# Kernel tuning notes

Measured on AMD Instinct MI355X. Metric: run time of the kernel, lower is better.

The kernel has to match this reference:

```python
import jax, jax.numpy as jnp
import numpy as np

B, D_IN, D, D_OUT, N_BLOCKS = 32768, 100, 1024, 1, 5
H = 0.1
EPS = 1e-4


def setup_inputs() -> dict:
    key = jax.random.key(0)
    ks = jax.random.split(key, 10)
    x = jax.random.normal(ks[0], (B, D_IN), dtype=jnp.float32)
    # first linear: D_IN -> D
    W0 = jax.random.normal(ks[1], (D, D_IN), dtype=jnp.float32) / np.sqrt(D_IN)
    b0 = jnp.zeros((D,), dtype=jnp.float32)
    # middle residual linears: D -> D, stacked over blocks
    Ws = jax.random.normal(ks[2], (N_BLOCKS, D, D), dtype=jnp.float32) / np.sqrt(D)
    bs = jnp.zeros((N_BLOCKS, D), dtype=jnp.float32)
    # brownian Linear(D, 1, bias=False) weight vectors, one per block
    bw = jax.random.normal(ks[3], (N_BLOCKS, D), dtype=jnp.float32) / np.sqrt(D)
    # last linear: D -> D_OUT
    Wlast = jax.random.normal(ks[4], (D_OUT, D), dtype=jnp.float32) / np.sqrt(D)
    blast = jnp.zeros((D_OUT,), dtype=jnp.float32)
    # torch.rand_like(out): uniform [0,1) noise per block
    noise = jax.random.uniform(ks[5], (N_BLOCKS, B, D), dtype=jnp.float32)
    return {"x": x, "W0": W0, "b0": b0, "Ws": Ws, "bs": bs,
            "bw": bw, "Wlast": Wlast, "blast": blast, "noise": noise}


def reference(x, W0, b0, Ws, bs, bw, Wlast, blast, noise):
    sqrt_h = H ** 0.5
    out = jnp.tanh(x @ W0.T + b0)  # [B, D]
    for i in range(N_BLOCKS):
        z = noise[i]  # [B, D]
        w = bw[i]     # [D]
        # product(): z @ (w w^T + eps I)^T = (z.w) w + eps z  (rank-1, O(D))
        proj = (z @ w)[:, None] * w + EPS * z
        out = out + H * jnp.tanh(out @ Ws[i].T + bs[i]) + sqrt_h * proj
    return out @ Wlast.T + blast  # [B, D_OUT]
```

## Files before the change

kernel.cpp:

```cpp
#include <hip/hip_runtime.h>
#include <hip/hip_bf16.h>


typedef unsigned short u16;
typedef __attribute__((ext_vector_type(8))) short short8;
typedef __attribute__((ext_vector_type(8))) u16 u16x8;
typedef __attribute__((ext_vector_type(4))) u16 u16x4;
typedef __attribute__((ext_vector_type(4))) float f32x4;

#define BROWS 32768
#define DDIM 1024
#define NBLK 5
#define H_STEP 0.1f
#define SQRT_H 0.31622776601683794f

#define FENCE() asm volatile("" ::: "memory")
#define BARRIER() do { FENCE(); __builtin_amdgcn_s_barrier(); FENCE(); } while (0)

__device__ __forceinline__ float bf2f(u16 u) {
    return __uint_as_float(((unsigned)u) << 16);
}
__device__ __forceinline__ u16 f2bf(float f) {
    unsigned u = __float_as_uint(f);
    unsigned r = 0x7fffu + ((u >> 16) & 1u);
    return (u16)((u + r) >> 16);
}
__device__ __forceinline__ float fast_tanh(float s) {
    float e = __expf(2.0f * s);
    return 1.0f - 2.0f * __builtin_amdgcn_rcpf(e + 1.0f);
}

#define GLOAD_LDS16(g, l)                                                        \
    __builtin_amdgcn_global_load_lds(                                            \
        (const __attribute__((address_space(1))) unsigned int*)(const void*)(g), \
        (__attribute__((address_space(3))) unsigned int*)(void*)(l), 16, 0, 0)

__global__ __launch_bounds__(256) void pad_cvt(const float* __restrict__ src,
                                               u16* __restrict__ dst,
                                               int R, int C, int Cp) {
    int idx = blockIdx.x * 256 + threadIdx.x;
    if (idx >= R * Cp) return;
    int r = idx / Cp;
    int c = idx - r * Cp;
    float v = (c < C) ? src[(size_t)r * C + c] : 0.0f;
    dst[idx] = f2bf(v);
}

__global__ __launch_bounds__(256) void zw_kernel(const float* __restrict__ noise,
                                                 const float* __restrict__ bw,
                                                 float* __restrict__ zw) {
    int gw = (blockIdx.x * 256 + threadIdx.x) >> 6;
    int lane = threadIdx.x & 63;
    if (gw >= NBLK * BROWS) return;
    int i = gw >> 15;
    const float* zr = noise + (size_t)gw * DDIM;
    const float* wr = bw + i * DDIM;
    float s = 0.0f;
#pragma unroll
    for (int it = 0; it < 4; ++it) {
        int k = it * 256 + lane * 4;
        f32x4 z = *(const f32x4*)(zr + k);
        f32x4 w = *(const f32x4*)(wr + k);
        s += z.x * w.x + z.y * w.y + z.z * w.z + z.w * w.w;
    }
#pragma unroll
    for (int off = 32; off > 0; off >>= 1) s += __shfl_down(s, off, 64);
    if (lane == 0) zw[gw] = s;
}

template <int KK, int EPI>
__global__ __launch_bounds__(512, 2) void gemm256(const u16* __restrict__ Ag,
                                                  const u16* __restrict__ Bg,
                                                  const float* __restrict__ bias,
                                                  u16* __restrict__ outW,
                                                  const u16* __restrict__ outR,
                                                  const float* __restrict__ zw,
                                                  const float* __restrict__ bwv) {
    constexpr int NT = KK / 64;
    static_assert(NT >= 2 && (NT & 1) == 0, "NT even, >=2");
    __shared__ __align__(16) u16 smem[65536];
    char* lds = (char*)smem;

    const int bid = blockIdx.x;
    const int swz = (bid & 7) * 64 + (bid >> 3);
    const int row0 = (swz >> 2) * 256;
    const int col0 = (swz & 3) * 256;

    const int tid = threadIdx.x;
    const int lane = tid & 63;
    const int wid = tid >> 6;
    const int wm = wid >> 2;
    const int wn = wid & 3;

    const int srow = tid >> 2;
    const int skq = (tid & 3) ^ ((tid >> 3) & 3);
    const u16* agp0 = Ag + (size_t)(row0 + srow) * KK + skq * 8;
    const u16* agp1 = Ag + (size_t)(row0 + 128 + srow) * KK + skq * 8;
    const u16* bgp0 = Bg + (size_t)(col0 + srow) * KK + skq * 8;
    const u16* bgp1 = Bg + (size_t)(col0 + 128 + srow) * KK + skq * 8;
    char* lp0 = lds + wid * 1024;

    auto stage = [&](int t, int q) {
        const int is_b = q & 1;
        const int kh = q >> 1;
        const int koff = t * 64 + kh * 32;
        char* dst = lp0 + ((t & 1) << 16) + (is_b << 15) + (kh << 14);
        const u16* g0 = (is_b ? bgp0 : agp0) + koff;
        const u16* g1 = (is_b ? bgp1 : agp1) + koff;
        GLOAD_LDS16(g0, dst);
        GLOAD_LDS16(g1, dst + 8192);
    };

    const int rchunk = ((lane >> 4) ^ ((lane >> 1) & 3)) << 4;
    const int aoffL = (wm * 128 + (lane & 15)) * 64 + rchunk;
    const int boffL = 32768 + (wn * 64 + (lane & 15)) * 64 + rchunk;

    short8 af[8], bf[4];
    f32x4 acc[8][4];
#pragma unroll
    for (int m = 0; m < 8; ++m)
#pragma unroll
        for (int n = 0; n < 4; ++n) acc[m][n] = (f32x4){0.f, 0.f, 0.f, 0.f};

#define RD(off) (*(const short8*)(lds + (off)))
#define PHASE2(kh, bufc, STG1, STG2, VMW)                                             \
    do {                                                                              \
        STG1;                                                                         \
        STG2;                                                                         \
        VMW;                                                                          \
        FENCE(); __builtin_amdgcn_s_barrier(); FENCE();                               \
        __builtin_amdgcn_s_setprio(1);                                                \
        const int rb = (bufc) * 65536 + (kh) * 16384;                                 \
        _Pragma("unroll") for (int m = 0; m < 8; ++m)                                 \
            af[m] = RD(rb + aoffL + m * 1024);                                        \
        _Pragma("unroll") for (int n = 0; n < 4; ++n)                                 \
            bf[n] = RD(rb + boffL + n * 1024);                                        \
        _Pragma("unroll") for (int m = 0; m < 8; ++m)                                 \
            _Pragma("unroll") for (int n = 0; n < 4; ++n)                             \
                acc[m][n] = __builtin_amdgcn_mfma_f32_16x16x32_bf16(af[m], bf[n], acc[m][n], 0, 0, 0); \
        __builtin_amdgcn_s_setprio(0);                                                \
        FENCE(); __builtin_amdgcn_s_barrier(); FENCE();                               \
    } while (0)
#define VM4 asm volatile("s_waitcnt vmcnt(4)" ::: "memory")
#define VM0 asm volatile("s_waitcnt vmcnt(0)" ::: "memory")
#define NOSTG ((void)0)
#define NOVM ((void)0)

#define TILE2(t, c)                                                                   \
    do {                                                                              \
        PHASE2(0, c, stage((t) + 1, 2), stage((t) + 1, 3), NOVM);                     \
        PHASE2(1, c, stage((t) + 2, 0), stage((t) + 2, 1), VM4);                      \
    } while (0)

    stage(0, 0); stage(0, 1); stage(0, 2); stage(0, 3);
    stage(1, 0); stage(1, 1);
    asm volatile("s_waitcnt vmcnt(4)" ::: "memory");
    BARRIER();

    for (int t2 = 0; t2 < NT / 2 - 1; ++t2) {
        TILE2(2 * t2, 0);
        TILE2(2 * t2 + 1, 1);
    }
    PHASE2(0, 0, stage(NT - 1, 2), stage(NT - 1, 3), NOVM);
    PHASE2(1, 0, NOSTG, NOSTG, VM0);
    PHASE2(0, 1, NOSTG, NOSTG, NOVM);
    PHASE2(1, 1, NOSTG, NOSTG, NOVM);

    float bcol[4];
#pragma unroll
    for (int ng = 0; ng < 4; ++ng) bcol[ng] = bias[col0 + wn * 64 + ng * 16 + (lane & 15)];

    char* wbase = lds + wid * 16384;
    const int lr0 = (lane >> 4) * 4;
    const int lc0 = lane & 15;
#pragma unroll
    for (int m = 0; m < 8; ++m) {
#pragma unroll
        for (int ng = 0; ng < 4; ++ng) {
#pragma unroll
            for (int j = 0; j < 4; ++j) {
                int lrow = m * 16 + lr0 + j;
                int lcol = ng * 16 + lc0;
                float t = fast_tanh(acc[m][ng][j] + bcol[ng]);
                float d = (EPI == 0) ? t : H_STEP * t;
                int chunk = (lcol >> 3) ^ ((lrow >> 2) & 7);
                *(u16*)(wbase + lrow * 128 + (chunk << 4) + (lcol & 7) * 2) = f2bf(d);
            }
        }
    }

    const int gr_base = row0 + wm * 128;
    const int gc_base = col0 + wn * 64;
#pragma unroll
    for (int it = 0; it < 16; ++it) {
        int lrow = it * 8 + (lane >> 3);
        int chunk = lane & 7;
        int schunk = chunk ^ ((lrow >> 2) & 7);
        u16x8 d8 = *(const u16x8*)(wbase + lrow * 128 + (schunk << 4));
        int grow = gr_base + lrow;
        int gcol = gc_base + chunk * 8;
        size_t gidx = (size_t)grow * DDIM + gcol;
        u16x8 o8;
        if constexpr (EPI == 0) {
            o8 = d8;
        } else {
            u16x8 old8 = *(const u16x8*)(outR + gidx);
            float zr = SQRT_H * zw[grow];
            f32x4 bw0 = *(const f32x4*)(bwv + gcol);
            f32x4 bw1 = *(const f32x4*)(bwv + gcol + 4);
#pragma unroll
            for (int e = 0; e < 8; ++e) {
                float bwe = (e < 4) ? bw0[e] : bw1[e - 4];
                float v = bf2f(old8[e]) + bf2f(d8[e]) + zr * bwe;
                o8[e] = f2bf(v);
            }
        }
        *(u16x8*)(outW + gidx) = o8;
    }
#undef RD
#undef PHASE2
#undef VM4
#undef VM0
#undef NOSTG
#undef NOVM
#undef TILE2
}

__global__ __launch_bounds__(256) void last_k(const u16* __restrict__ out,
                                              const float* __restrict__ wlast,
                                              const float* __restrict__ blast,
                                              float* __restrict__ y) {
    int gw = (blockIdx.x * 256 + threadIdx.x) >> 6;
    int lane = threadIdx.x & 63;
    if (gw >= BROWS) return;
    const u16* orow = out + (size_t)gw * DDIM;
    float s = 0.0f;
#pragma unroll
    for (int it = 0; it < 4; ++it) {
        int k = it * 256 + lane * 4;
        u16x4 o = *(const u16x4*)(orow + k);
        f32x4 w = *(const f32x4*)(wlast + k);
        s += bf2f(o.x) * w.x + bf2f(o.y) * w.y + bf2f(o.z) * w.z + bf2f(o.w) * w.w;
    }
#pragma unroll
    for (int off = 32; off > 0; off >>= 1) s += __shfl_down(s, off, 64);
    if (lane == 0) y[gw] = s + blast[0];
}

extern "C" void kernel_launch(void* const* d_in, const int* in_sizes, int n_in,
                              void* d_out, int out_size, void* d_ws, size_t ws_size,
                              hipStream_t stream) {
    const float* x     = (const float*)d_in[0];
    const float* W0    = (const float*)d_in[1];
    const float* b0    = (const float*)d_in[2];
    const float* Ws    = (const float*)d_in[3];
    const float* bs    = (const float*)d_in[4];
    const float* bw    = (const float*)d_in[5];
    const float* Wlast = (const float*)d_in[6];
    const float* blast = (const float*)d_in[7];
    const float* noise = (const float*)d_in[8];
    float* y = (float*)d_out;
    (void)in_sizes; (void)n_in; (void)out_size; (void)ws_size;

    char* ws = (char*)d_ws;
    size_t off = 0;
    auto alloc = [&](size_t bytes) {
        char* p = ws + off;
        off += (bytes + 255) & ~(size_t)255;
        return p;
    };
    u16* outB0 = (u16*)alloc((size_t)BROWS * DDIM * 2);
    u16* outB1 = (u16*)alloc((size_t)BROWS * DDIM * 2);
    u16* xb    = (u16*)alloc((size_t)BROWS * 128 * 2);
    u16* W0b   = (u16*)alloc((size_t)DDIM * 128 * 2);
    u16* Wsb   = (u16*)alloc((size_t)NBLK * DDIM * DDIM * 2);
    float* zw  = (float*)alloc((size_t)NBLK * BROWS * 4);

    pad_cvt<<<(BROWS * 128 + 255) / 256, 256, 0, stream>>>(x, xb, BROWS, 100, 128);
    pad_cvt<<<(DDIM * 128 + 255) / 256, 256, 0, stream>>>(W0, W0b, DDIM, 100, 128);
    pad_cvt<<<(NBLK * DDIM * DDIM + 255) / 256, 256, 0, stream>>>(Ws, Wsb, NBLK * DDIM, DDIM, DDIM);

    zw_kernel<<<(NBLK * BROWS) / 4, 256, 0, stream>>>(noise, bw, zw);

    gemm256<128, 0><<<512, 512, 0, stream>>>(xb, W0b, b0, outB0,
                                             nullptr, nullptr, nullptr);

    u16* cur = outB0;
    u16* nxt = outB1;
    for (int i = 0; i < NBLK; ++i) {
        gemm256<1024, 1><<<512, 512, 0, stream>>>(
            cur, Wsb + (size_t)i * DDIM * DDIM, bs + (size_t)i * DDIM, nxt, cur,
            zw + (size_t)i * BROWS, bw + (size_t)i * DDIM);
        u16* t = cur; cur = nxt; nxt = t;
    }

    last_k<<<BROWS / 4, 256, 0, stream>>>(cur, Wlast, blast, y);
}
```

Before: 605.8 us.

## Switch GEMM to 32x32x16 MFMA with fragment-contiguous LDS staging layout

Replaces the 16x16x32 bf16 MFMA inner loop with 32x32x16 MFMA tiles (4x2 per wave). It also restages global-to-LDS loads so each 32-row by 16-k fragment sits contiguously, letting each lane read its operand with one linear offset and no swizzle math. This cuts the number of MFMA issues and LDS reads per k-step, aiming for higher matrix-core throughput. The trade-off is a changed LDS layout with possible bank conflicts and a remapped epilogue indexing that must match the 32x32 accumulator layout.

```diff
diff --git a/kernel.cpp b/kernel.cpp
--- a/kernel.cpp
+++ b/kernel.cpp
@@ -7,6 +7,7 @@
 typedef __attribute__((ext_vector_type(8))) u16 u16x8;
 typedef __attribute__((ext_vector_type(4))) u16 u16x4;
 typedef __attribute__((ext_vector_type(4))) float f32x4;
+typedef __attribute__((ext_vector_type(16))) float f32x16;
 
 #define BROWS 32768
 #define DDIM 1024
@@ -92,96 +93,122 @@
     const int wm = wid >> 2;
     const int wn = wid & 3;
 
-    const int srow = tid >> 2;
-    const int skq = (tid & 3) ^ ((tid >> 3) & 3);
-    const u16* agp0 = Ag + (size_t)(row0 + srow) * KK + skq * 8;
-    const u16* agp1 = Ag + (size_t)(row0 + 128 + srow) * KK + skq * 8;
-    const u16* bgp0 = Bg + (size_t)(col0 + srow) * KK + skq * 8;
-    const u16* bgp1 = Bg + (size_t)(col0 + 128 + srow) * KK + skq * 8;
-    char* lp0 = lds + wid * 1024;
-
-    auto stage = [&](int t, int q) {
-        const int is_b = q & 1;
-        const int kh = q >> 1;
-        const int koff = t * 64 + kh * 32;
-        char* dst = lp0 + ((t & 1) << 16) + (is_b << 15) + (kh << 14);
-        const u16* g0 = (is_b ? bgp0 : agp0) + koff;
-        const u16* g1 = (is_b ? bgp1 : agp1) + koff;
-        GLOAD_LDS16(g0, dst);
-        GLOAD_LDS16(g1, dst + 8192);
+    const int lr = lane & 31;
+    const int lk = (lane >> 5) * 8;
+    const u16* aBase = Ag + (size_t)(row0 + lr) * KK + lk;
+    const u16* bBase = Bg + (size_t)(col0 + lr) * KK + lk;
+
+    auto stageQ = [&](int t, int kh, int j) {
+        const int q = j * 8 + wid;
+        const int isB = q >> 4;
+        const int qq = q & 15;
+        const int Mn = qq >> 1;
+        const int ks = kh * 2 + (qq & 1);
+        const u16* g = (isB ? bBase : aBase) + (size_t)Mn * 32 * KK + t * 64 + ks * 16;
+        char* dst = lds + ((t & 1) << 16) + (isB << 15) + (Mn * 4 + ks) * 1024;
+        GLOAD_LDS16(g, dst);
     };
 
-    const int rchunk = ((lane >> 4) ^ ((lane >> 1) & 3)) << 4;
-    const int aoffL = (wm * 128 + (lane & 15)) * 64 + rchunk;
-    const int boffL = 32768 + (wn * 64 + (lane & 15)) * 64 + rchunk;
-
-    short8 af[8], bf[4];
-    f32x4 acc[8][4];
-#pragma unroll
-    for (int m = 0; m < 8; ++m)
-#pragma unroll
-        for (int n = 0; n < 4; ++n) acc[m][n] = (f32x4){0.f, 0.f, 0.f, 0.f};
-
-#define RD(off) (*(const short8*)(lds + (off)))
-#define PHASE2(kh, bufc, STG1, STG2, VMW)                                             \
+    const int l16 = lane * 16;
+    const int aA0 = l16 + (wm << 14);
+    const int aA1 = aA0 + 65536;
+    const int bA0 = l16 + 32768 + (wn << 13);
+    const int bA1 = bA0 + 65536;
+
+    f32x16 acc[4][2];
+#pragma unroll
+    for (int mt = 0; mt < 4; ++mt)
+#pragma unroll
+        for (int nt = 0; nt < 2; ++nt)
+#pragma unroll
+            for (int e = 0; e < 16; ++e) acc[mt][nt][e] = 0.f;
+
+#define RDA(bufc, imm) (*(const short8*)(lds + ((bufc) ? aA1 : aA0) + (imm)))
+#define RDB(bufc, imm) (*(const short8*)(lds + ((bufc) ? bA1 : bA0) + (imm)))
+#define PHASE32(kh, bufc, STGS, VMW)                                                  \
     do {                                                                              \
-        STG1;                                                                         \
-        STG2;                                                                         \
+        STGS;                                                                         \
         VMW;                                                                          \
         FENCE(); __builtin_amdgcn_s_barrier(); FENCE();                               \
         __builtin_amdgcn_s_setprio(1);                                                \
-        const int rb = (bufc) * 65536 + (kh) * 16384;                                 \
-        _Pragma("unroll") for (int m = 0; m < 8; ++m)                                 \
-            af[m] = RD(rb + aoffL + m * 1024);                                        \
-        _Pragma("unroll") for (int n = 0; n < 4; ++n)                                 \
-            bf[n] = RD(rb + boffL + n * 1024);                                        \
-        _Pragma("unroll") for (int m = 0; m < 8; ++m)                                 \
-            _Pragma("unroll") for (int n = 0; n < 4; ++n)                             \
-                acc[m][n] = __builtin_amdgcn_mfma_f32_16x16x32_bf16(af[m], bf[n], acc[m][n], 0, 0, 0); \
+        short8 a0k0 = RDA(bufc, (0 * 4 + (kh) * 2 + 0) * 1024);                       \
+        short8 a1k0 = RDA(bufc, (1 * 4 + (kh) * 2 + 0) * 1024);                       \
+        short8 a2k0 = RDA(bufc, (2 * 4 + (kh) * 2 + 0) * 1024);                       \
+        short8 a3k0 = RDA(bufc, (3 * 4 + (kh) * 2 + 0) * 1024);                       \
+        short8 b0k0 = RDB(bufc, (0 * 4 + (kh) * 2 + 0) * 1024);                       \
+        short8 b1k0 = RDB(bufc, (1 * 4 + (kh) * 2 + 0) * 1024);                       \
+        short8 a0k1 = RDA(bufc, (0 * 4 + (kh) * 2 + 1) * 1024);                       \
+        short8 a1k1 = RDA(bufc, (1 * 4 + (kh) * 2 + 1) * 1024);                       \
+        short8 a2k1 = RDA(bufc, (2 * 4 + (kh) * 2 + 1) * 1024);                       \
+        short8 a3k1 = RDA(bufc, (3 * 4 + (kh) * 2 + 1) * 1024);                       \
+        short8 b0k1 = RDB(bufc, (0 * 4 + (kh) * 2 + 1) * 1024);                       \
+        short8 b1k1 = RDB(bufc, (1 * 4 + (kh) * 2 + 1) * 1024);                       \
+        acc[0][0] = __builtin_amdgcn_mfma_f32_32x32x16_bf16(a0k0, b0k0, acc[0][0], 0, 0, 0); \
+        acc[0][1] = __builtin_amdgcn_mfma_f32_32x32x16_bf16(a0k0, b1k0, acc[0][1], 0, 0, 0); \
+        acc[1][0] = __builtin_amdgcn_mfma_f32_32x32x16_bf16(a1k0, b0k0, acc[1][0], 0, 0, 0); \
+        acc[1][1] = __builtin_amdgcn_mfma_f32_32x32x16_bf16(a1k0, b1k0, acc[1][1], 0, 0, 0); \
+        acc[2][0] = __builtin_amdgcn_mfma_f32_32x32x16_bf16(a2k0, b0k0, acc[2][0], 0, 0, 0); \
+        acc[2][1] = __builtin_amdgcn_mfma_f32_32x32x16_bf16(a2k0, b1k0, acc[2][1], 0, 0, 0); \
+        acc[3][0] = __builtin_amdgcn_mfma_f32_32x32x16_bf16(a3k0, b0k0, acc[3][0], 0, 0, 0); \
+        acc[3][1] = __builtin_amdgcn_mfma_f32_32x32x16_bf16(a3k0, b1k0, acc[3][1], 0, 0, 0); \
+        acc[0][0] = __builtin_amdgcn_mfma_f32_32x32x16_bf16(a0k1, b0k1, acc[0][0], 0, 0, 0); \
+        acc[0][1] = __builtin_amdgcn_mfma_f32_32x32x16_bf16(a0k1, b1k1, acc[0][1], 0, 0, 0); \
+        acc[1][0] = __builtin_amdgcn_mfma_f32_32x32x16_bf16(a1k1, b0k1, acc[1][0], 0, 0, 0); \
+        acc[1][1] = __builtin_amdgcn_mfma_f32_32x32x16_bf16(a1k1, b1k1, acc[1][1], 0, 0, 0); \
+        acc[2][0] = __builtin_amdgcn_mfma_f32_32x32x16_bf16(a2k1, b0k1, acc[2][0], 0, 0, 0); \
+        acc[2][1] = __builtin_amdgcn_mfma_f32_32x32x16_bf16(a2k1, b1k1, acc[2][1], 0, 0, 0); \
+        acc[3][0] = __builtin_amdgcn_mfma_f32_32x32x16_bf16(a3k1, b0k1, acc[3][0], 0, 0, 0); \
+        acc[3][1] = __builtin_amdgcn_mfma_f32_32x32x16_bf16(a3k1, b1k1, acc[3][1], 0, 0, 0); \
         __builtin_amdgcn_s_setprio(0);                                                \
         FENCE(); __builtin_amdgcn_s_barrier(); FENCE();                               \
     } while (0)
+#define STG4(t, kh) do { stageQ(t, kh, 0); stageQ(t, kh, 1); stageQ(t, kh, 2); stageQ(t, kh, 3); } while (0)
 #define VM4 asm volatile("s_waitcnt vmcnt(4)" ::: "memory")
 #define VM0 asm volatile("s_waitcnt vmcnt(0)" ::: "memory")
 #define NOSTG ((void)0)
 #define NOVM ((void)0)
 
-#define TILE2(t, c)                                                                   \
+#define TILE32(t, c)                                                                  \
     do {                                                                              \
-        PHASE2(0, c, stage((t) + 1, 2), stage((t) + 1, 3), NOVM);                     \
-        PHASE2(1, c, stage((t) + 2, 0), stage((t) + 2, 1), VM4);                      \
+        PHASE32(0, c, STG4((t) + 1, 1), NOVM);                                        \
+        PHASE32(1, c, STG4((t) + 2, 0), VM4);                                         \
     } while (0)
 
-    stage(0, 0); stage(0, 1); stage(0, 2); stage(0, 3);
-    stage(1, 0); stage(1, 1);
+    STG4(0, 0); STG4(0, 1);
+    STG4(1, 0);
     asm volatile("s_waitcnt vmcnt(4)" ::: "memory");
     BARRIER();
 
     for (int t2 = 0; t2 < NT / 2 - 1; ++t2) {
-        TILE2(2 * t2, 0);
-        TILE2(2 * t2 + 1, 1);
-    }
-    PHASE2(0, 0, stage(NT - 1, 2), stage(NT - 1, 3), NOVM);
-    PHASE2(1, 0, NOSTG, NOSTG, VM0);
-    PHASE2(0, 1, NOSTG, NOSTG, NOVM);
-    PHASE2(1, 1, NOSTG, NOSTG, NOVM);
-
-    float bcol[4];
-#pragma unroll
-    for (int ng = 0; ng < 4; ++ng) bcol[ng] = bias[col0 + wn * 64 + ng * 16 + (lane & 15)];
+        TILE32(2 * t2, 0);
+        TILE32(2 * t2 + 1, 1);
+    }
+    PHASE32(0, 0, STG4(NT - 1, 1), NOVM);
+    PHASE32(1, 0, NOSTG, VM0);
+    PHASE32(0, 1, NOSTG, NOVM);
+    PHASE32(1, 1, NOSTG, NOVM);
+
+    float bcol[2], bwc[2];
+#pragma unroll
+    for (int nt = 0; nt < 2; ++nt) {
+        int cg = col0 + wn * 64 + nt * 32 + (lane & 31);
+        bcol[nt] = bias[cg];
+        if constexpr (EPI == 1) bwc[nt] = bwv[cg];
+    }
+    (void)bwc;
 
     char* wbase = lds + wid * 16384;
-    const int lr0 = (lane >> 4) * 4;
-    const int lc0 = lane & 15;
-#pragma unroll
-    for (int m = 0; m < 8; ++m) {
-#pragma unroll
-        for (int ng = 0; ng < 4; ++ng) {
-#pragma unroll
-            for (int j = 0; j < 4; ++j) {
-                int lrow = m * 16 + lr0 + j;
-                int lcol = ng * 16 + lc0;
-                float t = fast_tanh(acc[m][ng][j] + bcol[ng]);
+    const int cb = lane & 31;
+    const int rq = (lane >> 5) * 4;
+#pragma unroll
+    for (int mt = 0; mt < 4; ++mt) {
+#pragma unroll
+        for (int nt = 0; nt < 2; ++nt) {
+#pragma unroll
+            for (int reg = 0; reg < 16; ++reg) {
+                int lrow = mt * 32 + (reg & 3) + 8 * (reg >> 2) + rq;
+                int lcol = nt * 32 + cb;
+                float t = fast_tanh(acc[mt][nt][reg] + bcol[nt]);
                 float d = (EPI == 0) ? t : H_STEP * t;
                 int chunk = (lcol >> 3) ^ ((lrow >> 2) & 7);
                 *(u16*)(wbase + lrow * 128 + (chunk << 4) + (lcol & 7) * 2) = f2bf(d);
@@ -217,13 +244,15 @@
         }
         *(u16x8*)(outW + gidx) = o8;
     }
-#undef RD
-#undef PHASE2
+#undef RDA
+#undef RDB
+#undef PHASE32
+#undef STG4
 #undef VM4
 #undef VM0
 #undef NOSTG
 #undef NOVM
-#undef TILE2
+#undef TILE32
 }
 
 __global__ __launch_bounds__(256) void last_k(const u16* __restrict__ out,
```

Measured after the change: 666.8 us. 10.1% more time.
